# Optimization experiments

Measured on AMD Instinct MI355X. Metric: run time of the kernel, lower is better.

## Reference

```python
import jax, jax.numpy as jnp
import numpy as np

C = 1024          # embed_dim
H = 16            # num_heads
D = C // H        # head_dim = 64
M = 64            # memory_size
HID = 4 * C       # mlp hidden
EPS = 1e-5


def _ln(x, g, b):
    mu = jnp.mean(x, axis=-1, keepdims=True)
    var = jnp.mean(jnp.square(x - mu), axis=-1, keepdims=True)
    return (x - mu) * jax.lax.rsqrt(var + EPS) * g + b


def setup_inputs() -> dict:
    key = jax.random.key(0)
    ks = jax.random.split(key, 16)
    s = 0.02
    return {
        'x': jax.random.normal(ks[0], (2, 2048, C), jnp.float32),
        'memory': jax.random.normal(ks[1], (1, M, C), jnp.float32),
        'ln1_g': jnp.ones((C,), jnp.float32),
        'ln1_b': jnp.zeros((C,), jnp.float32),
        'w_qkv': jax.random.normal(ks[2], (C, 3 * C), jnp.float32) * s,
        'b_qkv': jnp.zeros((3 * C,), jnp.float32),
        'w_out': jax.random.normal(ks[3], (C, C), jnp.float32) * s,
        'b_out': jnp.zeros((C,), jnp.float32),
        'w_mem': jax.random.normal(ks[4], (C, C), jnp.float32) * s,
        'b_mem': jnp.zeros((C,), jnp.float32),
        'ln2_g': jnp.ones((C,), jnp.float32),
        'ln2_b': jnp.zeros((C,), jnp.float32),
        'w_fc1': jax.random.normal(ks[5], (C, HID), jnp.float32) * s,
        'b_fc1': jnp.zeros((HID,), jnp.float32),
        'w_fc2': jax.random.normal(ks[6], (HID, C), jnp.float32) * s,
        'b_fc2': jnp.zeros((C,), jnp.float32),
    }


def reference(x, memory, ln1_g, ln1_b, w_qkv, b_qkv, w_out, b_out,
              w_mem, b_mem, ln2_g, ln2_b, w_fc1, b_fc1, w_fc2, b_fc2):
    B, T, _ = x.shape
    scale = 1.0 / np.sqrt(D)

    # --- InfiniAttention on norm1(x) ---
    h = _ln(x, ln1_g, ln1_b)
    qkv = (h @ w_qkv + b_qkv).reshape(B, T, 3, H, D)
    q = qkv[:, :, 0].transpose(0, 2, 1, 3)  # (B,H,T,D)
    k = qkv[:, :, 1].transpose(0, 2, 1, 3)
    v = qkv[:, :, 2].transpose(0, 2, 1, 3)

    # local full softmax attention over the window of T tokens
    attn = jax.nn.softmax(jnp.einsum('bhtd,bhsd->bhts', q, k) * scale, axis=-1)
    local_out = jnp.einsum('bhts,bhsd->bhtd', attn, v)

    # compressive memory read: mem acts as both K and V
    mem = (memory @ w_mem + b_mem)                 # (1,M,C)
    mem_kv = jnp.broadcast_to(mem, (B, M, C)).reshape(B, M, H, D).transpose(0, 2, 1, 3)  # (B,H,M,D)
    mem_attn = jax.nn.softmax(jnp.einsum('bhtd,bhmd->bhtm', q, mem_kv) * scale, axis=-1)
    mem_out = jnp.einsum('bhtm,bhmd->bhtd', mem_attn, mem_kv)

    out = (local_out + mem_out).transpose(0, 2, 1, 3).reshape(B, T, C)
    out = out @ w_out + b_out
    x = x + out

    # --- MLP on norm2(x) ---
    h2 = _ln(x, ln2_g, ln2_b)
    h2 = jax.nn.gelu(h2 @ w_fc1 + b_fc1, approximate=False)
    x = x + h2 @ w_fc2 + b_fc2
    return x
```

## Files before the change

kernel.cpp:

```cpp
#include <hip/hip_runtime.h>
#include <hip/hip_bf16.h>

typedef unsigned short u16;
typedef unsigned int u32;
typedef short bf16x8 __attribute__((ext_vector_type(8)));
typedef float f32x4 __attribute__((ext_vector_type(4)));

__device__ __forceinline__ u16 f2bf(float x) {
    u32 u = __float_as_uint(x);
    u32 rounding = 0x7FFFu + ((u >> 16) & 1u);
    return (u16)((u + rounding) >> 16);
}

__device__ __forceinline__ void gload_lds16(const u16* g, u16* l) {
    __builtin_amdgcn_global_load_lds((const __attribute__((address_space(1))) void*)g,
                                     (__attribute__((address_space(3))) void*)l, 16, 0, 0);
}

__device__ __forceinline__ int xcd_swz(int id, int nwg) {
    int q = nwg >> 3, r = nwg & 7;
    int x = id & 7, k = id >> 3;
    return (x < r ? x * (q + 1) : r * (q + 1) + (x - r) * q) + k;
}

__global__ __launch_bounds__(256) void ln_kernel(const float* __restrict__ in,
                                                 const float* __restrict__ g,
                                                 const float* __restrict__ b,
                                                 u16* __restrict__ outp) {
    int tok = blockIdx.x;
    int t = threadIdx.x;
    const float4* row = (const float4*)(in + (size_t)tok * 1024);
    float4 v = row[t];
    float s = v.x + v.y + v.z + v.w;
    float sq = v.x * v.x + v.y * v.y + v.z * v.z + v.w * v.w;
#pragma unroll
    for (int off = 32; off >= 1; off >>= 1) {
        s += __shfl_xor(s, off);
        sq += __shfl_xor(sq, off);
    }
    __shared__ float rs[4], rq[4];
    int lane = t & 63, w = t >> 6;
    if (lane == 0) { rs[w] = s; rq[w] = sq; }
    __syncthreads();
    s = rs[0] + rs[1] + rs[2] + rs[3];
    sq = rq[0] + rq[1] + rq[2] + rq[3];
    float mean = s * (1.0f / 1024.0f);
    float var = sq * (1.0f / 1024.0f) - mean * mean;
    float rstd = rsqrtf(var + 1e-5f);
    float4 gg = ((const float4*)g)[t];
    float4 bb = ((const float4*)b)[t];
    u16* o = outp + (size_t)tok * 1024 + t * 4;
    o[0] = f2bf((v.x - mean) * rstd * gg.x + bb.x);
    o[1] = f2bf((v.y - mean) * rstd * gg.y + bb.y);
    o[2] = f2bf((v.z - mean) * rstd * gg.z + bb.z);
    o[3] = f2bf((v.w - mean) * rstd * gg.w + bb.w);
}

__global__ __launch_bounds__(256) void transpose_w(const float* __restrict__ W,
                                                   u16* __restrict__ WT, int K, int N) {
    __shared__ float tile[32][33];
    int n0 = blockIdx.x * 32, k0 = blockIdx.y * 32;
    int tx = threadIdx.x & 31, ty = threadIdx.x >> 5;
#pragma unroll
    for (int i = 0; i < 4; i++) {
        int kk = ty + i * 8;
        tile[kk][tx] = W[(size_t)(k0 + kk) * N + n0 + tx];
    }
    __syncthreads();
#pragma unroll
    for (int i = 0; i < 4; i++) {
        int nn = ty + i * 8;
        WT[(size_t)(n0 + nn) * K + k0 + tx] = f2bf(tile[tx][nn]);
    }
}

__global__ void convert_bf(const float* __restrict__ in, u16* __restrict__ outp, int n) {
    int i = blockIdx.x * blockDim.x + threadIdx.x;
    if (i < n) outp[i] = f2bf(in[i]);
}

__global__ __launch_bounds__(256) void prep_kv(const u16* __restrict__ src,
                                               u32* __restrict__ kdst, u32* __restrict__ vdst,
                                               long bstride, int rstride, int koff, int voff) {
    int t = blockIdx.x, bh = blockIdx.y;
    int b = bh >> 4, h = bh & 15;
    int tid = threadIdx.x;
    const u16* kS = src + (size_t)b * bstride + (size_t)(t * 64) * rstride + koff + h * 64;
    const u16* vS = src + (size_t)b * bstride + (size_t)(t * 64) * rstride + voff + h * 64;
    u32* kD = kdst + ((size_t)bh * gridDim.x + t) * 2048;
    u32* vD = vdst + ((size_t)bh * gridDim.x + t) * 2048;
#pragma unroll
    for (int c = 0; c < 2; c++) {
        int idx = tid + c * 256;
        int row = idx >> 3, blk = idx & 7;
        uint4 q = *(const uint4*)&kS[(size_t)row * rstride + blk * 8];
        *(uint4*)&kD[row * 32 + ((blk ^ (row & 7)) << 2)] = q;
    }
#pragma unroll
    for (int c = 0; c < 2; c++) {
        int idx = tid + c * 256;
        int drow = idx >> 3, kblk = idx & 7;
        u32 vv[4];
#pragma unroll
        for (int e = 0; e < 4; e++) {
            int j0 = kblk * 8 + 2 * e, j1 = j0 + 1;
            int kv0 = 16 * (j0 & 3) + (j0 >> 2);
            int kv1 = 16 * (j1 & 3) + (j1 >> 2);
            vv[e] = (u32)vS[(size_t)kv0 * rstride + drow] |
                    ((u32)vS[(size_t)kv1 * rstride + drow] << 16);
        }
        *(uint4*)&vD[drow * 32 + ((kblk ^ (drow & 7)) << 2)] = *(uint4*)vv;
    }
}

template <int MODE, int BM>
__global__ __launch_bounds__(256) void gemm_bf16(const u16* A, const u16* BT,
                                                 const float* __restrict__ bias,
                                                 const float* res, void* outv,
                                                 int M, int N, int K) {
    __shared__ __align__(16) u16 As[BM * 32];
    __shared__ __align__(16) u16 Bs[128 * 32];
    constexpr int MI = BM / 32;
    int gx = gridDim.x, gy = gridDim.y;
    int id = blockIdx.y * gx + blockIdx.x;
    int id2 = xcd_swz(id, gx * gy);
    int bx = id2 / gy, by = id2 % gy;
    int rowBase = by * BM, colBase = bx * 128;
    int t = threadIdx.x, lane = t & 63, w = t >> 6;
    int wr = w >> 1, wc = w & 1, r = lane & 15, g = lane >> 4;

    int lrow = lane >> 2;
    int scol = (lane & 3) * 8;
    const u16* b0 = BT + (size_t)(colBase + (w * 2 + 0) * 16 + lrow) * K + scol;
    const u16* b1 = BT + (size_t)(colBase + (w * 2 + 1) * 16 + lrow) * K + scol;
    u16* lB0 = &Bs[(w * 2 + 0) * 512];
    u16* lB1 = &Bs[(w * 2 + 1) * 512];
    const u16* a0;
    const u16* a1 = nullptr;
    u16 *lA0, *lA1 = nullptr;
    if constexpr (BM == 128) {
        a0 = A + (size_t)(rowBase + (w * 2 + 0) * 16 + lrow) * K + scol;
        a1 = A + (size_t)(rowBase + (w * 2 + 1) * 16 + lrow) * K + scol;
        lA0 = &As[(w * 2 + 0) * 512];
        lA1 = &As[(w * 2 + 1) * 512];
    } else {
        a0 = A + (size_t)(rowBase + w * 16 + lrow) * K + scol;
        lA0 = &As[w * 512];
    }

    f32x4 acc[MI][4] = {};

    for (int k0 = 0; k0 < K; k0 += 32) {
        __syncthreads();
        gload_lds16(a0 + k0, lA0);
        if constexpr (BM == 128) gload_lds16(a1 + k0, lA1);
        gload_lds16(b0 + k0, lB0);
        gload_lds16(b1 + k0, lB1);
        __syncthreads();
        bf16x8 af[MI], bfr[4];
#pragma unroll
        for (int mi = 0; mi < MI; mi++)
            af[mi] = *(const bf16x8*)&As[(wr * (BM / 2) + mi * 16 + r) * 32 + g * 8];
#pragma unroll
        for (int ni = 0; ni < 4; ni++)
            bfr[ni] = *(const bf16x8*)&Bs[(wc * 64 + ni * 16 + r) * 32 + g * 8];
#pragma unroll
        for (int mi = 0; mi < MI; mi++)
#pragma unroll
            for (int ni = 0; ni < 4; ni++)
                acc[mi][ni] = __builtin_amdgcn_mfma_f32_16x16x32_bf16(af[mi], bfr[ni], acc[mi][ni], 0, 0, 0);
    }

#pragma unroll
    for (int mi = 0; mi < MI; mi++) {
#pragma unroll
        for (int ni = 0; ni < 4; ni++) {
#pragma unroll
            for (int rr = 0; rr < 4; rr++) {
                int grow = rowBase + wr * (BM / 2) + mi * 16 + g * 4 + rr;
                int gcol = colBase + wc * 64 + ni * 16 + r;
                if (grow < M) {
                    float v = acc[mi][ni][rr] + bias[gcol];
                    if constexpr (MODE == 1) {
                        v = 0.5f * v * (1.0f + erff(v * 0.70710678118f));
                    }
                    if constexpr (MODE == 2) {
                        ((float*)outv)[(size_t)grow * N + gcol] = v + res[(size_t)grow * N + gcol];
                    } else {
                        ((u16*)outv)[(size_t)grow * N + gcol] = f2bf(v);
                    }
                }
            }
        }
    }
}

__global__ __launch_bounds__(256) void attn_kernel(const u16* __restrict__ qkv,
                                                   const u32* __restrict__ ktiled,
                                                   const u32* __restrict__ vttiled,
                                                   const u32* __restrict__ memK,
                                                   const u32* __restrict__ memVT,
                                                   u16* __restrict__ outp) {
    __shared__ __align__(16) u32 KB[2][2048];
    __shared__ __align__(16) u32 VB[2][2048];
    __shared__ __align__(16) u32 P32[64][32];
    const int T = 2048, C3 = 3072;
    int id = blockIdx.y * 32 + blockIdx.x;
    int id2 = xcd_swz(id, 1024);
    int bh = id2 >> 5, qt = id2 & 31;
    int b = bh >> 4, h = bh & 15;
    int t0 = qt * 64;
    int tid = threadIdx.x, lane = tid & 63, w = tid >> 6, r = lane & 15, g = lane >> 4;
    int swz = r & 7;
    size_t qkvb = (size_t)b * T * C3;

    const u16* qrow = qkv + qkvb + (size_t)(t0 + w * 16 + r) * C3 + h * 64;
    bf16x8 aq0 = *(const bf16x8*)(qrow + g * 8);
    bf16x8 aq1 = *(const bf16x8*)(qrow + 32 + g * 8);
#pragma unroll
    for (int i = 0; i < 8; i++) {
        float f0 = __uint_as_float(((u32)(u16)aq0[i]) << 16) * 0.18033688f;
        float f1 = __uint_as_float(((u32)(u16)aq1[i]) << 16) * 0.18033688f;
        aq0[i] = (short)f2bf(f0);
        aq1[i] = (short)f2bf(f1);
    }

    f32x4 O[4] = {};
    float m_[4] = {-1e30f, -1e30f, -1e30f, -1e30f};
    float lv[4] = {0.f, 0.f, 0.f, 0.f};

    auto stage = [&](int t, int buf) {
        const u32 *kb, *vb;
        if (t < 32) {
            kb = ktiled + ((size_t)bh * 32 + t) * 2048;
            vb = vttiled + ((size_t)bh * 32 + t) * 2048;
        } else {
            kb = memK + (size_t)h * 2048;
            vb = memVT + (size_t)h * 2048;
        }
        gload_lds16((const u16*)(kb + tid * 4), (u16*)&KB[buf][tid * 4]);
        gload_lds16((const u16*)(kb + 1024 + tid * 4), (u16*)&KB[buf][1024 + tid * 4]);
        gload_lds16((const u16*)(vb + tid * 4), (u16*)&VB[buf][tid * 4]);
        gload_lds16((const u16*)(vb + 1024 + tid * 4), (u16*)&VB[buf][1024 + tid * 4]);
    };

    auto compute = [&](int buf) {
        f32x4 sv[4];
#pragma unroll
        for (int n = 0; n < 4; n++) {
            int row = n * 16 + r;
            bf16x8 bk0 = *(const bf16x8*)&KB[buf][row * 32 + ((g ^ swz) << 2)];
            bf16x8 bk1 = *(const bf16x8*)&KB[buf][row * 32 + (((4 + g) ^ swz) << 2)];
            f32x4 z = {0.f, 0.f, 0.f, 0.f};
            z = __builtin_amdgcn_mfma_f32_16x16x32_bf16(aq0, bk0, z, 0, 0, 0);
            z = __builtin_amdgcn_mfma_f32_16x16x32_bf16(aq1, bk1, z, 0, 0, 0);
            sv[n] = z;
        }
        float mxl[4];
#pragma unroll
        for (int rr = 0; rr < 4; rr++)
            mxl[rr] = fmaxf(fmaxf(sv[0][rr], sv[1][rr]), fmaxf(sv[2][rr], sv[3][rr]));
        float dmax = fmaxf(fmaxf(mxl[0] - m_[0], mxl[1] - m_[1]),
                           fmaxf(mxl[2] - m_[2], mxl[3] - m_[3]));
        if (!__all(dmax <= 8.0f)) {
#pragma unroll
            for (int rr = 0; rr < 4; rr++) {
                float mxr = mxl[rr];
#pragma unroll
                for (int off = 8; off >= 1; off >>= 1) mxr = fmaxf(mxr, __shfl_xor(mxr, off));
                float mn = fmaxf(m_[rr], mxr);
                float alpha = exp2f(m_[rr] - mn);
                m_[rr] = mn;
                lv[rr] *= alpha;
#pragma unroll
                for (int n = 0; n < 4; n++) O[n][rr] *= alpha;
            }
        }
#pragma unroll
        for (int rr = 0; rr < 4; rr++) {
            int q = w * 16 + g * 4 + rr;
            float p0 = exp2f(sv[0][rr] - m_[rr]);
            float p1 = exp2f(sv[1][rr] - m_[rr]);
            float p2 = exp2f(sv[2][rr] - m_[rr]);
            float p3 = exp2f(sv[3][rr] - m_[rr]);
            lv[rr] += (p0 + p1) + (p2 + p3);
            uint2 pw;
            pw.x = __builtin_amdgcn_perm(__float_as_uint(p1), __float_as_uint(p0), 0x07060302u);
            pw.y = __builtin_amdgcn_perm(__float_as_uint(p3), __float_as_uint(p2), 0x07060302u);
            *(uint2*)&P32[q][4 * ((r >> 1) ^ (q & 7)) + 2 * (r & 1)] = pw;
        }
        bf16x8 ap0 = *(const bf16x8*)&P32[w * 16 + r][(g ^ swz) << 2];
        bf16x8 ap1 = *(const bf16x8*)&P32[w * 16 + r][((4 + g) ^ swz) << 2];
#pragma unroll
        for (int n = 0; n < 4; n++) {
            int row = n * 16 + r;
            bf16x8 bv0 = *(const bf16x8*)&VB[buf][row * 32 + ((g ^ swz) << 2)];
            bf16x8 bv1 = *(const bf16x8*)&VB[buf][row * 32 + (((4 + g) ^ swz) << 2)];
            O[n] = __builtin_amdgcn_mfma_f32_16x16x32_bf16(ap0, bv0, O[n], 0, 0, 0);
            O[n] = __builtin_amdgcn_mfma_f32_16x16x32_bf16(ap1, bv1, O[n], 0, 0, 0);
        }
    };

    float outLocal[4][4];
    stage(0, 0);
    __syncthreads();
    for (int tt = 0; tt <= 32; tt++) {
        if (tt < 32) stage(tt + 1, (tt + 1) & 1);
        if (tt == 32) {
#pragma unroll
            for (int rr = 0; rr < 4; rr++) {
                float ls = lv[rr];
#pragma unroll
                for (int off = 8; off >= 1; off >>= 1) ls += __shfl_xor(ls, off);
                float inv = 1.0f / ls;
#pragma unroll
                for (int n = 0; n < 4; n++) outLocal[n][rr] = O[n][rr] * inv;
                m_[rr] = -1e30f;
                lv[rr] = 0.f;
            }
#pragma unroll
            for (int n = 0; n < 4; n++) { f32x4 z = {0.f, 0.f, 0.f, 0.f}; O[n] = z; }
        }
        compute(tt & 1);
        __syncthreads();
    }
#pragma unroll
    for (int rr = 0; rr < 4; rr++) {
        float ls = lv[rr];
#pragma unroll
        for (int off = 8; off >= 1; off >>= 1) ls += __shfl_xor(ls, off);
        float inv = 1.0f / ls;
        int row = t0 + w * 16 + g * 4 + rr;
#pragma unroll
        for (int n = 0; n < 4; n++) {
            float v2 = outLocal[n][rr] + O[n][rr] * inv;
            outp[((size_t)(b * T + row)) * 1024 + h * 64 + n * 16 + r] = f2bf(v2);
        }
    }
}

extern "C" void kernel_launch(void* const* d_in, const int* in_sizes, int n_in,
                              void* d_out, int out_size, void* d_ws, size_t ws_size,
                              hipStream_t stream) {
    const float* x      = (const float*)d_in[0];
    const float* memory = (const float*)d_in[1];
    const float* ln1_g  = (const float*)d_in[2];
    const float* ln1_b  = (const float*)d_in[3];
    const float* w_qkv  = (const float*)d_in[4];
    const float* b_qkv  = (const float*)d_in[5];
    const float* w_out  = (const float*)d_in[6];
    const float* b_out  = (const float*)d_in[7];
    const float* w_mem  = (const float*)d_in[8];
    const float* b_mem  = (const float*)d_in[9];
    const float* ln2_g  = (const float*)d_in[10];
    const float* ln2_b  = (const float*)d_in[11];
    const float* w_fc1  = (const float*)d_in[12];
    const float* b_fc1  = (const float*)d_in[13];
    const float* w_fc2  = (const float*)d_in[14];
    const float* b_fc2  = (const float*)d_in[15];
    float* out = (float*)d_out;

    char* ws = (char*)d_ws;
    size_t off = 0;
    auto alloc = [&](size_t bytes) { size_t o = off; off += (bytes + 255) & ~(size_t)255; return o; };
    u16* h_bf    = (u16*)(ws + alloc((size_t)4096 * 1024 * 2));
    u16* qkv_bf  = (u16*)(ws + alloc((size_t)4096 * 3072 * 2));
    u16* attn_bf = (u16*)(ws + alloc((size_t)4096 * 1024 * 2));
    u16* g1_bf   = (u16*)(ws + alloc((size_t)4096 * 4096 * 2));
    u16* mem_bf  = (u16*)(ws + alloc((size_t)64 * 1024 * 2));
    u16* memA_bf = (u16*)(ws + alloc((size_t)64 * 1024 * 2));
    u16* wqkvT   = (u16*)(ws + alloc((size_t)3072 * 1024 * 2));
    u16* woutT   = (u16*)(ws + alloc((size_t)1024 * 1024 * 2));
    u16* wmemT   = (u16*)(ws + alloc((size_t)1024 * 1024 * 2));
    u16* wfc1T   = (u16*)(ws + alloc((size_t)4096 * 1024 * 2));
    u16* wfc2T   = (u16*)(ws + alloc((size_t)1024 * 4096 * 2));

    u32* ktiled  = (u32*)g1_bf;
    u32* vttiled = ktiled + (size_t)1024 * 2048;
    u32* memK    = vttiled + (size_t)1024 * 2048;
    u32* memVT   = memK + (size_t)16 * 2048;

    transpose_w<<<dim3(3072 / 32, 1024 / 32), 256, 0, stream>>>(w_qkv, wqkvT, 1024, 3072);
    transpose_w<<<dim3(1024 / 32, 1024 / 32), 256, 0, stream>>>(w_out, woutT, 1024, 1024);
    transpose_w<<<dim3(1024 / 32, 1024 / 32), 256, 0, stream>>>(w_mem, wmemT, 1024, 1024);
    transpose_w<<<dim3(4096 / 32, 1024 / 32), 256, 0, stream>>>(w_fc1, wfc1T, 1024, 4096);
    transpose_w<<<dim3(1024 / 32, 4096 / 32), 256, 0, stream>>>(w_fc2, wfc2T, 4096, 1024);
    convert_bf<<<dim3(256), 256, 0, stream>>>(memory, memA_bf, 64 * 1024);

    ln_kernel<<<dim3(4096), 256, 0, stream>>>(x, ln1_g, ln1_b, h_bf);

    gemm_bf16<0, 128><<<dim3(24, 32), 256, 0, stream>>>(h_bf, wqkvT, b_qkv, nullptr, qkv_bf, 4096, 3072, 1024);

    gemm_bf16<0, 64><<<dim3(8, 1), 256, 0, stream>>>(memA_bf, wmemT, b_mem, nullptr, mem_bf, 64, 1024, 1024);

    prep_kv<<<dim3(32, 32), 256, 0, stream>>>(qkv_bf, ktiled, vttiled,
                                              (long)2048 * 3072, 3072, 1024, 2048);
    prep_kv<<<dim3(1, 16), 256, 0, stream>>>(mem_bf, memK, memVT, 0, 1024, 0, 0);

    attn_kernel<<<dim3(32, 32), 256, 0, stream>>>(qkv_bf, ktiled, vttiled, memK, memVT, attn_bf);

    gemm_bf16<2, 64><<<dim3(8, 64), 256, 0, stream>>>(attn_bf, woutT, b_out, x, out, 4096, 1024, 1024);

    ln_kernel<<<dim3(4096), 256, 0, stream>>>(out, ln2_g, ln2_b, h_bf);

    gemm_bf16<1, 128><<<dim3(32, 32), 256, 0, stream>>>(h_bf, wfc1T, b_fc1, nullptr, g1_bf, 4096, 4096, 1024);

    gemm_bf16<2, 64><<<dim3(8, 64), 256, 0, stream>>>(g1_bf, wfc2T, b_fc2, out, out, 4096, 1024, 4096);

    (void)in_sizes; (void)n_in; (void)out_size; (void)ws_size;
}
```

Before: 493.5 us.

## Double-buffer LDS tiles in bf16 GEMM to overlap loads with MFMA

The GEMM main loop now uses two LDS buffers for the A and B tiles. It prefetches the next K-tile with global_load_lds while MFMAs run on the current tile, and needs only one barrier per iteration instead of two. It also raises wave priority around the MFMA block with s_setprio. This doubles LDS use per block, which may lower occupancy. The barrier placement relies on the compiler's waitcnt handling for the asynchronous LDS loads before the next read.

```diff
diff --git a/kernel.cpp b/kernel.cpp
--- a/kernel.cpp
+++ b/kernel.cpp
@@ -118,8 +118,8 @@
                                                  const float* __restrict__ bias,
                                                  const float* res, void* outv,
                                                  int M, int N, int K) {
-    __shared__ __align__(16) u16 As[BM * 32];
-    __shared__ __align__(16) u16 Bs[128 * 32];
+    __shared__ __align__(16) u16 As[2][BM * 32];
+    __shared__ __align__(16) u16 Bs[2][128 * 32];
     constexpr int MI = BM / 32;
     int gx = gridDim.x, gy = gridDim.y;
     int id = blockIdx.y * gx + blockIdx.x;
@@ -133,42 +133,51 @@
     int scol = (lane & 3) * 8;
     const u16* b0 = BT + (size_t)(colBase + (w * 2 + 0) * 16 + lrow) * K + scol;
     const u16* b1 = BT + (size_t)(colBase + (w * 2 + 1) * 16 + lrow) * K + scol;
-    u16* lB0 = &Bs[(w * 2 + 0) * 512];
-    u16* lB1 = &Bs[(w * 2 + 1) * 512];
+    int lB0 = (w * 2 + 0) * 512;
+    int lB1 = (w * 2 + 1) * 512;
     const u16* a0;
     const u16* a1 = nullptr;
-    u16 *lA0, *lA1 = nullptr;
+    int lA0, lA1 = 0;
     if constexpr (BM == 128) {
         a0 = A + (size_t)(rowBase + (w * 2 + 0) * 16 + lrow) * K + scol;
         a1 = A + (size_t)(rowBase + (w * 2 + 1) * 16 + lrow) * K + scol;
-        lA0 = &As[(w * 2 + 0) * 512];
-        lA1 = &As[(w * 2 + 1) * 512];
+        lA0 = (w * 2 + 0) * 512;
+        lA1 = (w * 2 + 1) * 512;
     } else {
         a0 = A + (size_t)(rowBase + w * 16 + lrow) * K + scol;
-        lA0 = &As[w * 512];
-    }
+        lA0 = w * 512;
+    }
+
+    auto stage = [&](int k0, int buf) {
+        gload_lds16(a0 + k0, &As[buf][lA0]);
+        if constexpr (BM == 128) gload_lds16(a1 + k0, &As[buf][lA1]);
+        gload_lds16(b0 + k0, &Bs[buf][lB0]);
+        gload_lds16(b1 + k0, &Bs[buf][lB1]);
+    };
 
     f32x4 acc[MI][4] = {};
-
-    for (int k0 = 0; k0 < K; k0 += 32) {
-        __syncthreads();
-        gload_lds16(a0 + k0, lA0);
-        if constexpr (BM == 128) gload_lds16(a1 + k0, lA1);
-        gload_lds16(b0 + k0, lB0);
-        gload_lds16(b1 + k0, lB1);
-        __syncthreads();
+    int nk = K >> 5;
+    stage(0, 0);
+    __syncthreads();
+    int cur = 0;
+    for (int kt = 0; kt < nk; kt++) {
+        if (kt + 1 < nk) stage((kt + 1) << 5, cur ^ 1);
         bf16x8 af[MI], bfr[4];
 #pragma unroll
         for (int mi = 0; mi < MI; mi++)
-            af[mi] = *(const bf16x8*)&As[(wr * (BM / 2) + mi * 16 + r) * 32 + g * 8];
+            af[mi] = *(const bf16x8*)&As[cur][(wr * (BM / 2) + mi * 16 + r) * 32 + g * 8];
 #pragma unroll
         for (int ni = 0; ni < 4; ni++)
-            bfr[ni] = *(const bf16x8*)&Bs[(wc * 64 + ni * 16 + r) * 32 + g * 8];
+            bfr[ni] = *(const bf16x8*)&Bs[cur][(wc * 64 + ni * 16 + r) * 32 + g * 8];
+        __builtin_amdgcn_s_setprio(1);
 #pragma unroll
         for (int mi = 0; mi < MI; mi++)
 #pragma unroll
             for (int ni = 0; ni < 4; ni++)
                 acc[mi][ni] = __builtin_amdgcn_mfma_f32_16x16x32_bf16(af[mi], bfr[ni], acc[mi][ni], 0, 0, 0);
+        __builtin_amdgcn_s_setprio(0);
+        __syncthreads();
+        cur ^= 1;
     }
 
 #pragma unroll
```

Measured after the change: 480.2 us. 2.7% less time.
